# Performance work log

Measured on AMD Instinct MI355X. Metric: run time of the kernel, lower is better.

## Reference

```python
import jax, jax.numpy as jnp
import numpy as np

N = 50000      # nodes
E = 800000     # edges
IN = 64        # in_channels
HID = 256      # hidden_dim
LAT = 64       # latent_dim
KS = 2         # kernel_size per dim
DIM = 3        # pseudo-coordinate dim
K = KS ** DIM  # 8 spline weight matrices


def spline_basis_coeffs(pseudo, ks, dim, dtype):
    """Degree-1 open B-spline basis: returns per-edge coefficients c [E, ks**dim]."""
    e = pseudo.shape[0]
    v = pseudo * (ks - 1)                                   # [E, dim]
    bot = jnp.clip(jnp.floor(v), 0, ks - 1).astype(jnp.int32)
    frac = v - bot
    c = jnp.zeros((e, ks ** dim), dtype)
    rows = jnp.arange(e)
    for s in range(2 ** dim):  # 8 knot combinations (fixed small loop)
        w = jnp.ones(e, dtype)
        idx = jnp.zeros(e, jnp.int32)
        for d in range(dim):
            bit = (s >> d) & 1
            w = w * (frac[:, d] if bit else 1.0 - frac[:, d])
            idx = idx + jnp.clip(bot[:, d] + bit, 0, ks - 1) * (ks ** d)
        c = c.at[rows, idx].add(w)
    return c


def spline_conv(x, edge_index, pseudo, W, Wroot, b):
    """SplineConv with aggr='mean', root weight and bias (degree-1 open splines)."""
    src, dst = edge_index[0], edge_index[1]
    n = x.shape[0]
    e = pseudo.shape[0]
    c = spline_basis_coeffs(pseudo, KS, DIM, x.dtype)        # [E, K]
    x_src = x[src]                                           # [E, in] gather
    deg = jax.ops.segment_sum(jnp.ones(e, x.dtype), dst, num_segments=n)
    inv_deg = (1.0 / jnp.maximum(deg, 1.0))[:, None]         # [N, 1] mean aggr
    out = jnp.zeros((n, W.shape[2]), x.dtype)
    for k in range(W.shape[0]):  # K=8 fixed loop; scatter-add then dense matmul
        agg = jax.ops.segment_sum(c[:, k:k + 1] * x_src, dst, num_segments=n)
        out = out + (agg * inv_deg) @ W[k]
    return out + x @ Wroot + b


def setup_inputs() -> dict:
    key = jax.random.key(0)
    ks = jax.random.split(key, 12)
    x = jax.random.normal(ks[0], (N, IN), jnp.float32)
    edge_index = jax.random.randint(ks[1], (2, E), 0, N, jnp.int32)
    s = 0.05
    return {
        "x": x,
        "edge_index": edge_index,
        "conv1_W": jax.random.normal(ks[2], (K, IN, HID), jnp.float32) * s,
        "conv1_root": jax.random.normal(ks[3], (IN, HID), jnp.float32) * s,
        "conv1_b": jnp.zeros((HID,), jnp.float32),
        "conv2_W": jax.random.normal(ks[4], (K, HID, LAT), jnp.float32) * s,
        "conv2_root": jax.random.normal(ks[5], (HID, LAT), jnp.float32) * s,
        "conv2_b": jnp.zeros((LAT,), jnp.float32),
        "dec_w1": jax.random.normal(ks[6], (LAT, HID), jnp.float32) * s,
        "dec_b1": jnp.zeros((HID,), jnp.float32),
        "dec_w2": jax.random.normal(ks[7], (HID, IN), jnp.float32) * s,
        "dec_b2": jnp.zeros((IN,), jnp.float32),
    }


def reference(x, edge_index, conv1_W, conv1_root, conv1_b,
              conv2_W, conv2_root, conv2_b,
              dec_w1, dec_b1, dec_w2, dec_b2):
    pseudo = jnp.zeros((edge_index.shape[1], DIM), x.dtype)  # forward builds zeros
    h = jax.nn.relu(spline_conv(x, edge_index, pseudo, conv1_W, conv1_root, conv1_b))
    z = spline_conv(h, edge_index, pseudo, conv2_W, conv2_root, conv2_b)
    h2 = jax.nn.relu(z @ dec_w1 + dec_b1)
    return h2 @ dec_w2 + dec_b2
```

## Files before the change

kernel.cpp:

```cpp
#include <hip/hip_runtime.h>
#include <hip/hip_bf16.h>


#define THREADS 256

typedef __attribute__((ext_vector_type(8))) short bf16x8;
typedef __attribute__((ext_vector_type(4))) float f32x4;

__device__ __forceinline__ float bf2f(unsigned short u) {
    unsigned v = ((unsigned)u) << 16;
    return __builtin_bit_cast(float, v);
}
__device__ __forceinline__ unsigned short f2bf(float f) {
    __hip_bfloat16 h = __float2bfloat16(f);
    return __builtin_bit_cast(unsigned short, h);
}

__device__ __forceinline__ void pack_one(unsigned short* dst,
                                         const float* W0, const float* W1,
                                         int NB, int ksplit, int colsplit,
                                         int ld0, int ld1, int t) {
    int i = t & 7, lane = (t >> 3) & 63, rest = t >> 9;
    int j = rest % NB, s = rest / NB;
    int k = s * 32 + ((lane >> 4) << 3) + i;
    int c = (j << 4) + (lane & 15);
    float v;
    if (c >= colsplit)    v = W1[(size_t)k * ld1 + (c - colsplit)];
    else if (k >= ksplit) v = W1[(size_t)(k - ksplit) * ld1 + c];
    else                  v = W0[(size_t)k * ld0 + c];
    dst[t] = f2bf(v);
}

#define BIG (1 << 30)

__global__ void prep_kernel(const float* __restrict__ W1g, const float* __restrict__ root1,
                            const float* __restrict__ W2g, const float* __restrict__ root2,
                            const float* __restrict__ dw1, const float* __restrict__ dw2,
                            const float* __restrict__ x, const int* __restrict__ dstv,
                            int* __restrict__ cnt,
                            unsigned short* __restrict__ Pb1,
                            unsigned short* __restrict__ Pb2,
                            unsigned short* __restrict__ Pd1,
                            unsigned short* __restrict__ Pd2,
                            unsigned short* __restrict__ ab1,
                            int n, int E) {
    int t = blockIdx.x * blockDim.x + threadIdx.x;
    if (t < 32768) {
        pack_one(Pb1, W1g, root1, 16, 64, BIG, 256, 256, t);
    } else if (t < 65536) {
        pack_one(Pb2, W2g, root2, 8, BIG, 64, 64, 64, t - 32768);
    } else if (t < 81920) {
        pack_one(Pd1, dw1, dw1, 16, BIG, BIG, 256, 256, t - 65536);
    } else if (t < 98304) {
        pack_one(Pd2, dw2, dw2, 4, BIG, BIG, 64, 64, t - 81920);
    } else if (t < 98304 + n * 64) {
        int u = t - 98304;
        int row = u >> 6, col = u & 63;
        ab1[(size_t)row * 128 + 64 + col] = f2bf(x[(size_t)row * 64 + col]);
    } else {
        int e = t - 98304 - n * 64;
        if (e < E) atomicAdd(&cnt[dstv[e]], 1);
    }
}

__global__ void scan_block(const int* __restrict__ cnt, int* __restrict__ offs,
                           int* __restrict__ bsum, int n) {
    __shared__ int tsum[256];
    int t = threadIdx.x;
    int base = blockIdx.x * 1024 + t * 4;
    int v0 = (base + 0 < n) ? cnt[base + 0] : 0;
    int v1 = (base + 1 < n) ? cnt[base + 1] : 0;
    int v2 = (base + 2 < n) ? cnt[base + 2] : 0;
    int v3 = (base + 3 < n) ? cnt[base + 3] : 0;
    int s = v0 + v1 + v2 + v3;
    tsum[t] = s;
    __syncthreads();
    for (int off = 1; off < 256; off <<= 1) {
        int xv = (t >= off) ? tsum[t - off] : 0;
        __syncthreads();
        tsum[t] += xv;
        __syncthreads();
    }
    int excl = tsum[t] - s;
    if (base + 0 < n) offs[base + 0] = excl;
    if (base + 1 < n) offs[base + 1] = excl + v0;
    if (base + 2 < n) offs[base + 2] = excl + v0 + v1;
    if (base + 3 < n) offs[base + 3] = excl + v0 + v1 + v2;
    if (t == 255) bsum[blockIdx.x] = tsum[255];
}

__global__ void scan_add2(int* __restrict__ offs, const int* __restrict__ bsum,
                          const int* __restrict__ cnt, float* __restrict__ invd,
                          int* __restrict__ bcur, int n, int sb) {
    __shared__ int sm[256];
    int t = threadIdx.x;
    sm[t] = (t < sb) ? bsum[t] : 0;
    __syncthreads();
    for (int off = 1; off < 256; off <<= 1) {
        int xv = (t >= off) ? sm[t - off] : 0;
        __syncthreads();
        sm[t] += xv;
        __syncthreads();
    }
    int i = blockIdx.x * blockDim.x + t;
    if (i < n) {
        int blk = i >> 10;
        int carry = blk ? sm[blk - 1] : 0;
        int v = offs[i] + carry;
        offs[i] = v;
        if ((i & 255) == 0) bcur[i >> 8] = v;
        invd[i] = 1.0f / (float)max(cnt[i], 1);
    }
    if (i == 0) offs[n] = sm[sb - 1];
}

__global__ __launch_bounds__(256) void partition_edges(
    const int* __restrict__ src, const int* __restrict__ dst,
    int* __restrict__ bcur, int* __restrict__ epack, int E) {
    __shared__ int hist[256];
    __shared__ int base[256];
    __shared__ int lcur[256];
    int t = threadIdx.x;
    hist[t] = 0;
    __syncthreads();
    int e0 = blockIdx.x * 4096;
    int myd[16], mys[16];
#pragma unroll
    for (int i = 0; i < 16; ++i) {
        int e = e0 + t + i * 256;
        int d = (e < E) ? dst[e] : -1;
        mys[i] = (e < E) ? src[e] : 0;
        myd[i] = d;
        if (d >= 0) atomicAdd(&hist[d >> 8], 1);
    }
    __syncthreads();
    int h = hist[t];
    if (h > 0) base[t] = atomicAdd(&bcur[t], h);
    lcur[t] = 0;
    __syncthreads();
#pragma unroll
    for (int i = 0; i < 16; ++i) {
        int d = myd[i];
        if (d >= 0) {
            int b = d >> 8;
            int p = atomicAdd(&lcur[b], 1);
            epack[base[b] + p] = ((d & 255) << 20) | mys[i];
        }
    }
}

__global__ __launch_bounds__(256) void bucket_fill(
    const int* __restrict__ epack, const int* __restrict__ offs,
    int* __restrict__ esrc, int N) {
    __shared__ int loff[257];
    __shared__ int ncur[256];
    __shared__ int stage[8192];
    int b = blockIdx.x, t = threadIdx.x;
    int n0 = b << 8;
    int cntn = min(256, N - n0);
    for (int i = t; i <= cntn; i += 256) loff[i] = offs[n0 + i];
    ncur[t] = 0;
    __syncthreads();
    int ebase = loff[0];
    int ecount = loff[cntn] - ebase;
    bool useLds = (ecount <= 8192);
    for (int i = t; i < ecount; i += 256) {
        int p = epack[ebase + i];
        int dl = p >> 20;
        int pos = atomicAdd(&ncur[dl], 1);
        int g = loff[dl] + pos;
        int sv = p & 0xFFFFF;
        if (useLds) stage[g - ebase] = sv;
        else        esrc[g] = sv;
    }
    __syncthreads();
    if (useLds)
        for (int i = t; i < ecount; i += 256) esrc[ebase + i] = stage[i];
}

__global__ void agg_x_pair(unsigned short* __restrict__ ab1, const int* __restrict__ esrc,
                           const int* __restrict__ offs, const float* __restrict__ invd,
                           int n) {
    int node = blockIdx.x * 4 + (threadIdx.x >> 6);
    if (node >= n) return;
    int l = threadIdx.x & 63;
    int slot = l >> 5, c = l & 31;
    const unsigned short* xb = ab1 + 64 + c * 2;
    int s = offs[node], e = offs[node + 1];
    float a0 = 0.f, a1 = 0.f, b0 = 0.f, b1 = 0.f;
    float c0 = 0.f, c1 = 0.f, d0 = 0.f, d1 = 0.f;
    int j = s;
    for (; j + 8 <= e; j += 8) {
        int i0 = esrc[j + slot], i1 = esrc[j + 2 + slot];
        int i2 = esrc[j + 4 + slot], i3 = esrc[j + 6 + slot];
        unsigned v0 = *(const unsigned*)(xb + (size_t)i0 * 128);
        unsigned v1 = *(const unsigned*)(xb + (size_t)i1 * 128);
        unsigned v2 = *(const unsigned*)(xb + (size_t)i2 * 128);
        unsigned v3 = *(const unsigned*)(xb + (size_t)i3 * 128);
        a0 += bf2f((unsigned short)v0); a1 += bf2f((unsigned short)(v0 >> 16));
        b0 += bf2f((unsigned short)v1); b1 += bf2f((unsigned short)(v1 >> 16));
        c0 += bf2f((unsigned short)v2); c1 += bf2f((unsigned short)(v2 >> 16));
        d0 += bf2f((unsigned short)v3); d1 += bf2f((unsigned short)(v3 >> 16));
    }
    for (; j + 2 <= e; j += 2) {
        int i0 = esrc[j + slot];
        unsigned v0 = *(const unsigned*)(xb + (size_t)i0 * 128);
        a0 += bf2f((unsigned short)v0); a1 += bf2f((unsigned short)(v0 >> 16));
    }
    if (j < e && slot == 0) {
        int i0 = esrc[j];
        unsigned v0 = *(const unsigned*)(xb + (size_t)i0 * 128);
        a0 += bf2f((unsigned short)v0); a1 += bf2f((unsigned short)(v0 >> 16));
    }
    float r0 = (a0 + b0) + (c0 + d0), r1 = (a1 + b1) + (c1 + d1);
    r0 += __shfl_xor(r0, 32);
    r1 += __shfl_xor(r1, 32);
    if (slot == 0) {
        float iv = invd[node];
        unsigned o = ((unsigned)f2bf(r1 * iv) << 16) | (unsigned)f2bf(r0 * iv);
        *(unsigned*)(ab1 + (size_t)node * 128 + c * 2) = o;
    }
}

__global__ void agg_z_pair(const unsigned short* __restrict__ hwroot,
                           const int* __restrict__ esrc, const int* __restrict__ offs,
                           const float* __restrict__ invd, const float* __restrict__ b2,
                           unsigned short* __restrict__ z, int n) {
    int node = blockIdx.x * 4 + (threadIdx.x >> 6);
    if (node >= n) return;
    int l = threadIdx.x & 63;
    int slot = l >> 5, c = l & 31;
    const unsigned short* hb = hwroot + c * 2;
    int s = offs[node], e = offs[node + 1];
    float a0 = 0.f, a1 = 0.f, b0 = 0.f, b1 = 0.f;
    float c0 = 0.f, c1 = 0.f, d0 = 0.f, d1 = 0.f;
    int j = s;
    for (; j + 8 <= e; j += 8) {
        int i0 = esrc[j + slot], i1 = esrc[j + 2 + slot];
        int i2 = esrc[j + 4 + slot], i3 = esrc[j + 6 + slot];
        unsigned v0 = *(const unsigned*)(hb + (size_t)i0 * 128);
        unsigned v1 = *(const unsigned*)(hb + (size_t)i1 * 128);
        unsigned v2 = *(const unsigned*)(hb + (size_t)i2 * 128);
        unsigned v3 = *(const unsigned*)(hb + (size_t)i3 * 128);
        a0 += bf2f((unsigned short)v0); a1 += bf2f((unsigned short)(v0 >> 16));
        b0 += bf2f((unsigned short)v1); b1 += bf2f((unsigned short)(v1 >> 16));
        c0 += bf2f((unsigned short)v2); c1 += bf2f((unsigned short)(v2 >> 16));
        d0 += bf2f((unsigned short)v3); d1 += bf2f((unsigned short)(v3 >> 16));
    }
    for (; j + 2 <= e; j += 2) {
        int i0 = esrc[j + slot];
        unsigned v0 = *(const unsigned*)(hb + (size_t)i0 * 128);
        a0 += bf2f((unsigned short)v0); a1 += bf2f((unsigned short)(v0 >> 16));
    }
    if (j < e && slot == 0) {
        int i0 = esrc[j];
        unsigned v0 = *(const unsigned*)(hb + (size_t)i0 * 128);
        a0 += bf2f((unsigned short)v0); a1 += bf2f((unsigned short)(v0 >> 16));
    }
    float r0 = (a0 + b0) + (c0 + d0), r1 = (a1 + b1) + (c1 + d1);
    r0 += __shfl_xor(r0, 32);
    r1 += __shfl_xor(r1, 32);
    if (slot == 0) {
        float iv = invd[node];
        unsigned hr = *(const unsigned*)(hwroot + (size_t)node * 128 + 64 + c * 2);
        float v0 = r0 * iv + bf2f((unsigned short)hr) + b2[c * 2];
        float v1 = r1 * iv + bf2f((unsigned short)(hr >> 16)) + b2[c * 2 + 1];
        unsigned o = ((unsigned)f2bf(v1) << 16) | (unsigned)f2bf(v0);
        *(unsigned*)(z + (size_t)node * 64 + c * 2) = o;
    }
}

template <int K1, int NBW2, bool OUTBF>
__global__ __launch_bounds__(256) void gemm_fused(
    const unsigned short* __restrict__ A,
    const unsigned short* __restrict__ Bp1, const float* __restrict__ bias1,
    const unsigned short* __restrict__ Bp2, const float* __restrict__ bias2,
    void* __restrict__ Cv, int n)
{
    constexpr int KS1 = K1 / 32;
    constexpr int N2 = NBW2 * 64;
    constexpr int NB2 = NBW2 * 4;
    __shared__ unsigned short ht[64][264];

    const int m0 = blockIdx.x * 64;
    const int lane = threadIdx.x & 63;
    const int w = threadIdx.x >> 6;
    const int quad = lane >> 4;
    const int l16 = lane & 15;

    {
        f32x4 acc[4][4] = {};
        const unsigned short* Arow = A + (size_t)(m0 + l16) * K1 + quad * 8;
        for (int s = 0; s < KS1; ++s) {
            bf16x8 a[4];
#pragma unroll
            for (int mb = 0; mb < 4; ++mb)
                a[mb] = *(const bf16x8*)(Arow + (size_t)mb * 16 * K1 + s * 32);
#pragma unroll
            for (int jn = 0; jn < 4; ++jn) {
                int j = w * 4 + jn;
                bf16x8 b = *(const bf16x8*)(Bp1 + ((size_t)(s * 16 + j) * 64 + lane) * 8);
#pragma unroll
                for (int mb = 0; mb < 4; ++mb)
                    acc[mb][jn] = __builtin_amdgcn_mfma_f32_16x16x32_bf16(a[mb], b, acc[mb][jn], 0, 0, 0);
            }
        }
#pragma unroll
        for (int jn = 0; jn < 4; ++jn) {
            int col = (w * 4 + jn) * 16 + l16;
            float bv = bias1[col];
#pragma unroll
            for (int mb = 0; mb < 4; ++mb)
#pragma unroll
                for (int r = 0; r < 4; ++r) {
                    int row = mb * 16 + quad * 4 + r;
                    ht[row][col] = f2bf(fmaxf(acc[mb][jn][r] + bv, 0.f));
                }
        }
    }
    __syncthreads();

    {
        f32x4 acc[4][NBW2] = {};
        for (int s = 0; s < 8; ++s) {
            bf16x8 a[4];
#pragma unroll
            for (int mb = 0; mb < 4; ++mb)
                a[mb] = *(const bf16x8*)&ht[mb * 16 + l16][s * 32 + quad * 8];
#pragma unroll
            for (int jn = 0; jn < NBW2; ++jn) {
                int j = w * NBW2 + jn;
                bf16x8 b = *(const bf16x8*)(Bp2 + ((size_t)(s * NB2 + j) * 64 + lane) * 8);
#pragma unroll
                for (int mb = 0; mb < 4; ++mb)
                    acc[mb][jn] = __builtin_amdgcn_mfma_f32_16x16x32_bf16(a[mb], b, acc[mb][jn], 0, 0, 0);
            }
        }
#pragma unroll
        for (int jn = 0; jn < NBW2; ++jn) {
            int col = (w * NBW2 + jn) * 16 + l16;
            float bv = bias2 ? bias2[col] : 0.f;
#pragma unroll
            for (int mb = 0; mb < 4; ++mb)
#pragma unroll
                for (int r = 0; r < 4; ++r) {
                    int row = m0 + mb * 16 + quad * 4 + r;
                    if (row < n) {
                        float v = acc[mb][jn][r] + bv;
                        if (OUTBF)
                            ((unsigned short*)Cv)[(size_t)row * N2 + col] = f2bf(v);
                        else
                            ((float*)Cv)[(size_t)row * N2 + col] = v;
                    }
                }
        }
    }
}

extern "C" void kernel_launch(void* const* d_in, const int* in_sizes, int n_in,
                              void* d_out, int out_size, void* d_ws, size_t ws_size,
                              hipStream_t stream) {
    const float* x      = (const float*)d_in[0];
    const int*   ei     = (const int*)d_in[1];
    const float* W1g    = (const float*)d_in[2];
    const float* root1  = (const float*)d_in[3];
    const float* b1     = (const float*)d_in[4];
    const float* W2g    = (const float*)d_in[5];
    const float* root2  = (const float*)d_in[6];
    const float* b2     = (const float*)d_in[7];
    const float* dw1    = (const float*)d_in[8];
    const float* db1    = (const float*)d_in[9];
    const float* dw2    = (const float*)d_in[10];
    const float* db2    = (const float*)d_in[11];
    float* out = (float*)d_out;

    const int N = in_sizes[0] / 64;
    const int E = in_sizes[1] / 2;
    const int Npad = N + 64;
    const int* srcv = ei;
    const int* dstv = ei + E;

    char* ws = (char*)d_ws;
    auto alloc = [&](size_t bytes) -> void* {
        void* p = (void*)ws;
        ws += (bytes + 255) & ~(size_t)255;
        return p;
    };
    int*   cnt    = (int*)alloc((size_t)N * 4);
    int*   offs   = (int*)alloc((size_t)(N + 1) * 4);
    int*   bsum   = (int*)alloc(1024);
    int*   bcur   = (int*)alloc(1024);
    float* invd   = (float*)alloc((size_t)N * 4);
    int*   esrc   = (int*)alloc((size_t)E * 4);
    int*   epack  = (int*)alloc((size_t)E * 4);
    unsigned short* Pb1 = (unsigned short*)alloc(32768 * 2);
    unsigned short* Pb2 = (unsigned short*)alloc(32768 * 2);
    unsigned short* Pd1 = (unsigned short*)alloc(16384 * 2);
    unsigned short* Pd2 = (unsigned short*)alloc(16384 * 2);
    unsigned short* ab1    = (unsigned short*)alloc((size_t)Npad * 128 * 2);
    unsigned short* hwroot = (unsigned short*)alloc((size_t)Npad * 128 * 2);
    unsigned short* z      = (unsigned short*)alloc((size_t)Npad * 64 * 2);

    hipMemsetAsync(cnt, 0, (size_t)N * 4, stream);

    int nb = (N + THREADS - 1) / THREADS;
    int sb = (N + 1023) / 1024;
    int gb = (N + 63) / 64;
    int pb = (98304 + N * 64 + E + THREADS - 1) / THREADS;
    int nbkt = (N + 255) / 256;
    int pa = (E + 4095) / 4096;

    prep_kernel<<<pb, THREADS, 0, stream>>>(W1g, root1, W2g, root2, dw1, dw2, x,
                                            dstv, cnt, Pb1, Pb2, Pd1, Pd2, ab1, N, E);
    scan_block<<<sb, 256, 0, stream>>>(cnt, offs, bsum, N);
    scan_add2<<<nb, THREADS, 0, stream>>>(offs, bsum, cnt, invd, bcur, N, sb);
    partition_edges<<<pa, 256, 0, stream>>>(srcv, dstv, bcur, epack, E);
    bucket_fill<<<nbkt, 256, 0, stream>>>(epack, offs, esrc, N);

    agg_x_pair<<<(N + 3) / 4, THREADS, 0, stream>>>(ab1, esrc, offs, invd, N);
    gemm_fused<128, 2, true><<<gb, 256, 0, stream>>>(ab1, Pb1, b1, Pb2, nullptr, hwroot, N);
    agg_z_pair<<<(N + 3) / 4, THREADS, 0, stream>>>(hwroot, esrc, offs, invd, b2, z, N);
    gemm_fused<64, 1, false><<<gb, 256, 0, stream>>>(z, Pd1, db1, Pd2, db2, out, N);
}
```

Measured before the change: 243.1 us.

## Replace per-node degree count and global scan with bucket histogram and local scan

Per-node degree counting with global atomics and a two-kernel prefix scan over all nodes is replaced by a per-block shared-memory histogram of 256-node buckets, a single-block scan over bucket counts, and a per-bucket local histogram and scan inside the fill kernel, which now writes node offsets and inverse degrees itself. This removes one kernel launch, the large-array global atomics, and a full scan pass over N, at the cost of re-reading the packed edges once more in the bucket fill kernel.

```diff
diff --git a/kernel.cpp b/kernel.cpp
--- a/kernel.cpp
+++ b/kernel.cpp
@@ -37,13 +37,29 @@
                             const float* __restrict__ W2g, const float* __restrict__ root2,
                             const float* __restrict__ dw1, const float* __restrict__ dw2,
                             const float* __restrict__ x, const int* __restrict__ dstv,
-                            int* __restrict__ cnt,
+                            int* __restrict__ bcnt,
                             unsigned short* __restrict__ Pb1,
                             unsigned short* __restrict__ Pb2,
                             unsigned short* __restrict__ Pd1,
                             unsigned short* __restrict__ Pd2,
                             unsigned short* __restrict__ ab1,
-                            int n, int E) {
+                            int n, int E, int pb_pack) {
+    if ((int)blockIdx.x >= pb_pack) {
+        __shared__ int hist[256];
+        int t = threadIdx.x;
+        hist[t] = 0;
+        __syncthreads();
+        int e0 = ((int)blockIdx.x - pb_pack) * 4096;
+#pragma unroll
+        for (int i = 0; i < 16; ++i) {
+            int e = e0 + t + i * 256;
+            if (e < E) atomicAdd(&hist[dstv[e] >> 8], 1);
+        }
+        __syncthreads();
+        int h = hist[t];
+        if (h) atomicAdd(&bcnt[t], h);
+        return;
+    }
     int t = blockIdx.x * blockDim.x + threadIdx.x;
     if (t < 32768) {
         pack_one(Pb1, W1g, root1, 16, 64, BIG, 256, 256, t);
@@ -57,44 +73,16 @@
         int u = t - 98304;
         int row = u >> 6, col = u & 63;
         ab1[(size_t)row * 128 + 64 + col] = f2bf(x[(size_t)row * 64 + col]);
-    } else {
-        int e = t - 98304 - n * 64;
-        if (e < E) atomicAdd(&cnt[dstv[e]], 1);
-    }
-}
-
-__global__ void scan_block(const int* __restrict__ cnt, int* __restrict__ offs,
-                           int* __restrict__ bsum, int n) {
-    __shared__ int tsum[256];
-    int t = threadIdx.x;
-    int base = blockIdx.x * 1024 + t * 4;
-    int v0 = (base + 0 < n) ? cnt[base + 0] : 0;
-    int v1 = (base + 1 < n) ? cnt[base + 1] : 0;
-    int v2 = (base + 2 < n) ? cnt[base + 2] : 0;
-    int v3 = (base + 3 < n) ? cnt[base + 3] : 0;
-    int s = v0 + v1 + v2 + v3;
-    tsum[t] = s;
-    __syncthreads();
-    for (int off = 1; off < 256; off <<= 1) {
-        int xv = (t >= off) ? tsum[t - off] : 0;
-        __syncthreads();
-        tsum[t] += xv;
-        __syncthreads();
-    }
-    int excl = tsum[t] - s;
-    if (base + 0 < n) offs[base + 0] = excl;
-    if (base + 1 < n) offs[base + 1] = excl + v0;
-    if (base + 2 < n) offs[base + 2] = excl + v0 + v1;
-    if (base + 3 < n) offs[base + 3] = excl + v0 + v1 + v2;
-    if (t == 255) bsum[blockIdx.x] = tsum[255];
-}
-
-__global__ void scan_add2(int* __restrict__ offs, const int* __restrict__ bsum,
-                          const int* __restrict__ cnt, float* __restrict__ invd,
-                          int* __restrict__ bcur, int n, int sb) {
+    }
+}
+
+__global__ void scan_buckets(const int* __restrict__ bcnt, int* __restrict__ bbase,
+                             int* __restrict__ bcur, int* __restrict__ offs,
+                             int nbkt, int N, int E) {
     __shared__ int sm[256];
     int t = threadIdx.x;
-    sm[t] = (t < sb) ? bsum[t] : 0;
+    int v = (t < nbkt) ? bcnt[t] : 0;
+    sm[t] = v;
     __syncthreads();
     for (int off = 1; off < 256; off <<= 1) {
         int xv = (t >= off) ? sm[t - off] : 0;
@@ -102,16 +90,10 @@
         sm[t] += xv;
         __syncthreads();
     }
-    int i = blockIdx.x * blockDim.x + t;
-    if (i < n) {
-        int blk = i >> 10;
-        int carry = blk ? sm[blk - 1] : 0;
-        int v = offs[i] + carry;
-        offs[i] = v;
-        if ((i & 255) == 0) bcur[i >> 8] = v;
-        invd[i] = 1.0f / (float)max(cnt[i], 1);
-    }
-    if (i == 0) offs[n] = sm[sb - 1];
+    int ex = sm[t] - v;
+    bbase[t] = ex;
+    bcur[t] = ex;
+    if (t == 0) { bbase[256] = E; offs[N] = E; }
 }
 
 __global__ __launch_bounds__(256) void partition_edges(
@@ -149,20 +131,41 @@
     }
 }
 
-__global__ __launch_bounds__(256) void bucket_fill(
-    const int* __restrict__ epack, const int* __restrict__ offs,
+__global__ __launch_bounds__(256) void bucket_fill2(
+    const int* __restrict__ epack, const int* __restrict__ bbase,
+    int* __restrict__ offs, float* __restrict__ invd,
     int* __restrict__ esrc, int N) {
-    __shared__ int loff[257];
+    __shared__ int nh[256];
+    __shared__ int loff[256];
     __shared__ int ncur[256];
     __shared__ int stage[8192];
     int b = blockIdx.x, t = threadIdx.x;
     int n0 = b << 8;
     int cntn = min(256, N - n0);
-    for (int i = t; i <= cntn; i += 256) loff[i] = offs[n0 + i];
+    int ebase = bbase[b];
+    int ecount = bbase[b + 1] - ebase;
+    nh[t] = 0;
+    __syncthreads();
+    for (int i = t; i < ecount; i += 256)
+        atomicAdd(&nh[epack[ebase + i] >> 20], 1);
+    __syncthreads();
+    int v = nh[t];
+    loff[t] = v;
+    __syncthreads();
+    for (int off = 1; off < 256; off <<= 1) {
+        int xv = (t >= off) ? loff[t - off] : 0;
+        __syncthreads();
+        loff[t] += xv;
+        __syncthreads();
+    }
+    int ex = loff[t] - v;
+    loff[t] = ex;
+    if (t < cntn) {
+        offs[n0 + t] = ebase + ex;
+        invd[n0 + t] = 1.0f / (float)max(v, 1);
+    }
     ncur[t] = 0;
     __syncthreads();
-    int ebase = loff[0];
-    int ecount = loff[cntn] - ebase;
     bool useLds = (ecount <= 8192);
     for (int i = t; i < ecount; i += 256) {
         int p = epack[ebase + i];
@@ -170,8 +173,8 @@
         int pos = atomicAdd(&ncur[dl], 1);
         int g = loff[dl] + pos;
         int sv = p & 0xFFFFF;
-        if (useLds) stage[g - ebase] = sv;
-        else        esrc[g] = sv;
+        if (useLds) stage[g] = sv;
+        else        esrc[ebase + g] = sv;
     }
     __syncthreads();
     if (useLds)
@@ -386,10 +389,10 @@
         ws += (bytes + 255) & ~(size_t)255;
         return p;
     };
-    int*   cnt    = (int*)alloc((size_t)N * 4);
+    int*   bcnt   = (int*)alloc(1024);
+    int*   bbase  = (int*)alloc(1056);
+    int*   bcur   = (int*)alloc(1024);
     int*   offs   = (int*)alloc((size_t)(N + 1) * 4);
-    int*   bsum   = (int*)alloc(1024);
-    int*   bcur   = (int*)alloc(1024);
     float* invd   = (float*)alloc((size_t)N * 4);
     int*   esrc   = (int*)alloc((size_t)E * 4);
     int*   epack  = (int*)alloc((size_t)E * 4);
@@ -401,21 +404,19 @@
     unsigned short* hwroot = (unsigned short*)alloc((size_t)Npad * 128 * 2);
     unsigned short* z      = (unsigned short*)alloc((size_t)Npad * 64 * 2);
 
-    hipMemsetAsync(cnt, 0, (size_t)N * 4, stream);
-
-    int nb = (N + THREADS - 1) / THREADS;
-    int sb = (N + 1023) / 1024;
+    hipMemsetAsync(bcnt, 0, 1024, stream);
+
     int gb = (N + 63) / 64;
-    int pb = (98304 + N * 64 + E + THREADS - 1) / THREADS;
     int nbkt = (N + 255) / 256;
     int pa = (E + 4095) / 4096;
-
-    prep_kernel<<<pb, THREADS, 0, stream>>>(W1g, root1, W2g, root2, dw1, dw2, x,
-                                            dstv, cnt, Pb1, Pb2, Pd1, Pd2, ab1, N, E);
-    scan_block<<<sb, 256, 0, stream>>>(cnt, offs, bsum, N);
-    scan_add2<<<nb, THREADS, 0, stream>>>(offs, bsum, cnt, invd, bcur, N, sb);
+    int pb_pack = (98304 + N * 64 + THREADS - 1) / THREADS;
+
+    prep_kernel<<<pb_pack + pa, THREADS, 0, stream>>>(
+        W1g, root1, W2g, root2, dw1, dw2, x, dstv, bcnt,
+        Pb1, Pb2, Pd1, Pd2, ab1, N, E, pb_pack);
+    scan_buckets<<<1, 256, 0, stream>>>(bcnt, bbase, bcur, offs, nbkt, N, E);
     partition_edges<<<pa, 256, 0, stream>>>(srcv, dstv, bcur, epack, E);
-    bucket_fill<<<nbkt, 256, 0, stream>>>(epack, offs, esrc, N);
+    bucket_fill2<<<nbkt, 256, 0, stream>>>(epack, bbase, offs, invd, esrc, N);
 
     agg_x_pair<<<(N + 3) / 4, THREADS, 0, stream>>>(ab1, esrc, offs, invd, N);
     gemm_fused<128, 2, true><<<gb, 256, 0, stream>>>(ab1, Pb1, b1, Pb2, nullptr, hwroot, N);
```

After: 212.9 us. 12.4% less time.
